# Kernel optimization log

Measured on AMD Instinct MI355X. Metric: run time of the kernel, lower is better.

## Reference

```python
import jax, jax.numpy as jnp
import numpy as np

N = 50000       # nodes
E = 500000      # edges
IN = 128        # in_channels
H = 128         # hidden_channels
R = 8           # num_relations


def setup_inputs() -> dict:
    key = jax.random.key(0)
    ks = jax.random.split(key, 12)
    s_in = 1.0 / np.sqrt(IN)
    s_h = 1.0 / np.sqrt(H)
    return {
        "x": jax.random.normal(ks[0], (N, IN), dtype=jnp.float32),
        "edge_index": jax.random.randint(ks[1], (2, E), 0, N),
        "edge_type": jax.random.randint(ks[2], (E,), 0, R),
        "W1": jax.random.normal(ks[3], (R, IN, H), dtype=jnp.float32) * s_in,
        "root1": jax.random.normal(ks[4], (IN, H), dtype=jnp.float32) * s_in,
        "b1": jnp.zeros((H,), dtype=jnp.float32),
        "W2": jax.random.normal(ks[5], (R, H, H), dtype=jnp.float32) * s_h,
        "root2": jax.random.normal(ks[6], (H, H), dtype=jnp.float32) * s_h,
        "b2": jnp.zeros((H,), dtype=jnp.float32),
        "Wc": jax.random.normal(ks[7], (H, 1), dtype=jnp.float32) * s_h,
        "bc": jnp.zeros((1,), dtype=jnp.float32),
    }


def rgcn_layer(x, W, root, bias, src, dst, etype, num_nodes):
    """PyG RGCNConv (no basis decomposition, aggr='mean', root weight + bias):
    out[i] = x[i] @ root + bias + sum_r mean_{(j->i) in rel r} x[j] @ W[r]
    """
    out = x @ root + bias
    for r in range(W.shape[0]):  # small fixed relation count
        mask = (etype == r).astype(x.dtype)          # [E]
        xr = x @ W[r]                                 # [N, out]
        msg = xr[src] * mask[:, None]                 # gather + mask, [E, out]
        s = jax.ops.segment_sum(msg, dst, num_segments=num_nodes)   # [N, out]
        cnt = jax.ops.segment_sum(mask, dst, num_segments=num_nodes)  # [N]
        out = out + s / jnp.maximum(cnt, 1.0)[:, None]
    return out


def reference(x, edge_index, edge_type, W1, root1, b1, W2, root2, b2, Wc, bc):
    src, dst = edge_index[0], edge_index[1]
    h = jax.nn.relu(rgcn_layer(x, W1, root1, b1, src, dst, edge_type, x.shape[0]))
    # dropout p=0.2 is identity in eval mode
    h = jax.nn.relu(rgcn_layer(h, W2, root2, b2, src, dst, edge_type, x.shape[0]))
    return (h @ Wc + bc)[:, 0]  # squeeze(-1) -> [N]
```

## Files before the change

### kernel.cpp

```cpp
#include <hip/hip_runtime.h>

#define Hd 128
#define LDA 136
#define ZW 1152
#define ZW2 576
#define MAXDEG 64

typedef __attribute__((ext_vector_type(8))) short short8;
typedef __attribute__((ext_vector_type(4))) float f32x4;
typedef __attribute__((ext_vector_type(4))) unsigned int u32x4;

__device__ __forceinline__ unsigned short f2bf(float f) {
    union { float f; unsigned u; } v; v.f = f;
    unsigned r = v.u + 0x7FFFu + ((v.u >> 16) & 1u);
    return (unsigned short)(r >> 16);
}

__global__ __launch_bounds__(256) void prep_kernel(const float* __restrict__ x,
                                                   unsigned short* __restrict__ xbf, int n4,
                                                   const float* __restrict__ root1,
                                                   const float* __restrict__ W1,
                                                   const float* __restrict__ root2,
                                                   const float* __restrict__ W2,
                                                   unsigned short* __restrict__ Bt,
                                                   const int* __restrict__ src,
                                                   const int* __restrict__ dstp,
                                                   const int* __restrict__ et, int E,
                                                   int* __restrict__ deg,
                                                   unsigned int* __restrict__ epk,
                                                   unsigned long long* __restrict__ ovf,
                                                   int* __restrict__ ovfc) {
    const int tid = threadIdx.x;
    if (blockIdx.x < 18) {
        __shared__ float S[32 * 129];
        const int b = blockIdx.x;
        const float* Ws;
        if (b == 0)       Ws = root1;
        else if (b < 9)   Ws = W1 + (size_t)(b - 1) * 16384;
        else if (b == 9)  Ws = root2;
        else              Ws = W2 + (size_t)(b - 10) * 16384;
        unsigned short* Bd = Bt + (size_t)b * 16384;
        for (int s = 0; s < 4; ++s) {
            __syncthreads();
#pragma unroll
            for (int i = 0; i < 16; ++i) {
                int idx = i * 256 + tid;
                int k = idx >> 7, n = idx & 127;
                S[k * 129 + n] = Ws[(size_t)(32 * s + k) * 128 + n];
            }
            __syncthreads();
#pragma unroll
            for (int i = 0; i < 16; ++i) {
                int idx = i * 256 + tid;
                int n = idx >> 5, kk = idx & 31;
                int k = 32 * s + kk;
                int kp = (b >= 9) ? (((k & 15) << 3) | (k >> 4)) : k;
                Bd[n * 128 + kp] = f2bf(S[kk * 129 + n]);
            }
        }
    } else if (blockIdx.x < 18 + 512) {
        const int stride = 512 * 256;
        for (int i = (blockIdx.x - 18) * 256 + tid; i < n4; i += stride) {
            float4 v = ((const float4*)x)[i];
            ushort4 o;
            o.x = f2bf(v.x); o.y = f2bf(v.y); o.z = f2bf(v.z); o.w = f2bf(v.w);
            ((ushort4*)xbf)[i] = o;
        }
    } else {
        int e = (blockIdx.x - 530) * 256 + tid;
        if (e < E) {
            int r = et[e];
            int d = dstp[e];
            int idx = atomicAdd(&deg[d], 1);
            unsigned pay = ((unsigned)src[e] << 3) | (unsigned)r;
            if (idx < MAXDEG) epk[(size_t)d * MAXDEG + idx] = pay;
            else {
                int o = atomicAdd(ovfc, 1);
                ovf[o] = ((unsigned long long)(unsigned)d << 32) | pay;
            }
        }
    }
}

__global__ __launch_bounds__(256, 3) void gemm_z(const unsigned short* __restrict__ A,
                                                 const unsigned short* __restrict__ Bt9,
                                                 unsigned short* __restrict__ z, int M) {
    __shared__ __align__(16) unsigned short As[128 * LDA];
    __shared__ __align__(16) unsigned short Bs[64 * LDA];
    const int tid = threadIdx.x;

    const int nwg = gridDim.x;
    const int nq = nwg >> 3, rr = nwg & 7;
    const int xcd = blockIdx.x & 7, bix = blockIdx.x >> 3;
    const int swz = (xcd < rr ? xcd * (nq + 1) : rr * (nq + 1) + (xcd - rr) * nq) + bix;
    const int mtile = swz / 9, ctile = swz % 9;

    const int rowBase = mtile * 128;
    const int wave = tid >> 6, lane = tid & 63;
    const int lm = lane & 15, lk = (lane >> 4) * 8;
    const unsigned short* Btt = Bt9 + (size_t)ctile * 16384;

#pragma unroll
    for (int i = 0; i < 8; ++i) {
        int idx = i * 256 + tid;
        int r = idx >> 4, c16 = idx & 15;
        int grow = rowBase + r; if (grow >= M) grow = M - 1;
        *(float4*)&As[r * LDA + c16 * 8] = *(const float4*)&A[(size_t)grow * Hd + c16 * 8];
    }
#pragma unroll
    for (int i = 0; i < 4; ++i) {
        int idx = i * 256 + tid;
        *(float4*)&Bs[(idx >> 4) * LDA + (idx & 15) * 8] = *(const float4*)&Btt[idx * 8];
    }

    f32x4 acc[2][8];
#pragma unroll
    for (int mt = 0; mt < 2; ++mt)
#pragma unroll
        for (int nt = 0; nt < 8; ++nt) acc[mt][nt] = (f32x4){0.f, 0.f, 0.f, 0.f};

    __syncthreads();
#pragma unroll
    for (int ks = 0; ks < 4; ++ks) {
        const int k0 = ks * 32 + lk;
        short8 af0 = *(const short8*)&As[(wave * 32 + lm) * LDA + k0];
        short8 af1 = *(const short8*)&As[(wave * 32 + 16 + lm) * LDA + k0];
#pragma unroll
        for (int nt = 0; nt < 4; ++nt) {
            short8 bf = *(const short8*)&Bs[(nt * 16 + lm) * LDA + k0];
            acc[0][nt] = __builtin_amdgcn_mfma_f32_16x16x32_bf16(af0, bf, acc[0][nt], 0, 0, 0);
            acc[1][nt] = __builtin_amdgcn_mfma_f32_16x16x32_bf16(af1, bf, acc[1][nt], 0, 0, 0);
        }
    }
    __syncthreads();
#pragma unroll
    for (int i = 0; i < 4; ++i) {
        int idx = i * 256 + tid;
        *(float4*)&Bs[(idx >> 4) * LDA + (idx & 15) * 8] = *(const float4*)&Btt[(1024 + idx) * 8];
    }
    __syncthreads();
#pragma unroll
    for (int ks = 0; ks < 4; ++ks) {
        const int k0 = ks * 32 + lk;
        short8 af0 = *(const short8*)&As[(wave * 32 + lm) * LDA + k0];
        short8 af1 = *(const short8*)&As[(wave * 32 + 16 + lm) * LDA + k0];
#pragma unroll
        for (int nt = 4; nt < 8; ++nt) {
            short8 bf = *(const short8*)&Bs[((nt - 4) * 16 + lm) * LDA + k0];
            acc[0][nt] = __builtin_amdgcn_mfma_f32_16x16x32_bf16(af0, bf, acc[0][nt], 0, 0, 0);
            acc[1][nt] = __builtin_amdgcn_mfma_f32_16x16x32_bf16(af1, bf, acc[1][nt], 0, 0, 0);
        }
    }

    const int rquad = (lane >> 4) * 4;
#pragma unroll
    for (int mt = 0; mt < 2; ++mt)
#pragma unroll
        for (int reg = 0; reg < 4; ++reg) {
            int row = rowBase + wave * 32 + mt * 16 + rquad + reg;
            if (row >= M) continue;
            u32x4 qv;
#pragma unroll
            for (int j = 0; j < 4; ++j) {
                unsigned lo = f2bf(acc[mt][2 * j][reg]);
                unsigned hi = f2bf(acc[mt][2 * j + 1][reg]);
                qv[j] = lo | (hi << 16);
            }
            *(u32x4*)((char*)z + (size_t)row * (ZW * 2) + ctile * 256 + lm * 16) = qv;
        }
}

__global__ __launch_bounds__(256) void gather_out(const unsigned short* __restrict__ z,
                                                  const int* __restrict__ deg,
                                                  const unsigned int* __restrict__ epk,
                                                  const unsigned long long* __restrict__ ovf,
                                                  const int* __restrict__ ovfc,
                                                  const float* __restrict__ bias,
                                                  const float* __restrict__ Wc,
                                                  const float* __restrict__ bc,
                                                  unsigned short* __restrict__ outb,
                                                  float* __restrict__ outf,
                                                  int N, int mode) {
    const int lane = threadIdx.x & 63;
    const int node = (int)((blockIdx.x * 256 + threadIdx.x) >> 6);
    if (node >= N) return;
    const unsigned int* z32 = (const unsigned int*)z;
    const int half = lane >> 5;
    const int q = lane & 31;

    uint2 vr = *(const uint2*)(z32 + (size_t)node * ZW2 + 2 * q);
    int dt = __builtin_amdgcn_readfirstlane(deg[node]);
    unsigned int ep_v = epk[(size_t)node * MAXDEG + lane];
    const int degc = (dt < MAXDEG) ? dt : MAXDEG;
    const int rel_l = (int)(ep_v & 7u);
    const bool valid = lane < degc;

    int cnt_l = 0;
#pragma unroll
    for (int r = 0; r < 8; ++r) {
        unsigned long long m = __ballot(valid && (rel_l == r));
        int c = (int)__popcll(m);
        if (lane == r) cnt_l = c;
    }
    if (dt > MAXDEG) {
        int oc = __builtin_amdgcn_readfirstlane(ovfc[0]);
        for (int j = 0; j < oc; ++j) {
            unsigned long long v = ovf[j];
            if ((int)(v >> 32) == node && lane == (int)(v & 7u)) cnt_l++;
        }
    }
    float winv = 1.0f / (float)((cnt_l < 1) ? 1 : cnt_l);

    float t0 = 0.f, t1 = 0.f, t2 = 0.f, t3 = 0.f;
#pragma unroll 1
    for (int g = 0; g < degc; g += 16) {
        uint2 vb[8];
        float wb[8];
#pragma unroll
        for (int k = 0; k < 8; ++k) {
            int i = g + 2 * k + half;
            int ic = (i < degc) ? i : (degc - 1);
            unsigned pk = (unsigned)__shfl((int)ep_v, ic);
            int rel = (int)(pk & 7u);
            unsigned base = (pk >> 3) * ZW2 + (unsigned)(rel + 1) * 64;
            vb[k] = *(const uint2*)(z32 + (size_t)base + 2 * q);
            wb[k] = (i < degc) ? __shfl(winv, rel) : 0.f;
        }
#pragma unroll
        for (int k = 0; k < 8; ++k) {
            t0 += wb[k] * __uint_as_float(vb[k].x << 16);
            t1 += wb[k] * __uint_as_float(vb[k].x & 0xffff0000u);
            t2 += wb[k] * __uint_as_float(vb[k].y << 16);
            t3 += wb[k] * __uint_as_float(vb[k].y & 0xffff0000u);
        }
    }
    if (dt > MAXDEG) {
        int oc = __builtin_amdgcn_readfirstlane(ovfc[0]);
        for (int j = 0; j < oc; ++j) {
            unsigned long long v = ovf[j];
            if ((int)(v >> 32) == node) {
                unsigned pk = (unsigned)(v & 0xffffffffu);
                int rel = (int)(pk & 7u);
                unsigned base = (pk >> 3) * ZW2 + (unsigned)(rel + 1) * 64;
                uint2 u = *(const uint2*)(z32 + (size_t)base + 2 * q);
                float w = __shfl(winv, rel);
                if (half == 0) {
                    t0 += w * __uint_as_float(u.x << 16);
                    t1 += w * __uint_as_float(u.x & 0xffff0000u);
                    t2 += w * __uint_as_float(u.y << 16);
                    t3 += w * __uint_as_float(u.y & 0xffff0000u);
                }
            }
        }
    }

    t0 += __shfl_xor(t0, 32);
    t1 += __shfl_xor(t1, 32);
    t2 += __shfl_xor(t2, 32);
    t3 += __shfl_xor(t3, 32);

    const int p0 = 4 * q;
    const int c0 = ((p0 & 7) << 4) + (p0 >> 3);
    const int c1 = (((p0 + 1) & 7) << 4) + ((p0 + 1) >> 3);
    const int c2 = (((p0 + 2) & 7) << 4) + ((p0 + 2) >> 3);
    const int c3 = (((p0 + 3) & 7) << 4) + ((p0 + 3) >> 3);

    t0 = fmaxf(t0 + __uint_as_float(vr.x << 16)         + bias[c0], 0.f);
    t1 = fmaxf(t1 + __uint_as_float(vr.x & 0xffff0000u) + bias[c1], 0.f);
    t2 = fmaxf(t2 + __uint_as_float(vr.y << 16)         + bias[c2], 0.f);
    t3 = fmaxf(t3 + __uint_as_float(vr.y & 0xffff0000u) + bias[c3], 0.f);

    if (mode == 1) {
        if (half == 0) {
            uint2 o;
            o.x = (unsigned)f2bf(t0) | ((unsigned)f2bf(t1) << 16);
            o.y = (unsigned)f2bf(t2) | ((unsigned)f2bf(t3) << 16);
            *(uint2*)((unsigned int*)outb + (size_t)node * 64 + 2 * q) = o;
        }
    } else {
        float s = t0 * Wc[c0] + t1 * Wc[c1] + t2 * Wc[c2] + t3 * Wc[c3];
        s += __shfl_xor(s, 1);
        s += __shfl_xor(s, 2);
        s += __shfl_xor(s, 4);
        s += __shfl_xor(s, 8);
        s += __shfl_xor(s, 16);
        if (lane == 0) outf[node] = s + bc[0];
    }
}

extern "C" void kernel_launch(void* const* d_in, const int* in_sizes, int n_in,
                              void* d_out, int out_size, void* d_ws, size_t ws_size,
                              hipStream_t stream) {
    const float* x     = (const float*)d_in[0];
    const int*   ei    = (const int*)d_in[1];
    const int*   et    = (const int*)d_in[2];
    const float* W1    = (const float*)d_in[3];
    const float* root1 = (const float*)d_in[4];
    const float* b1    = (const float*)d_in[5];
    const float* W2    = (const float*)d_in[6];
    const float* root2 = (const float*)d_in[7];
    const float* b2    = (const float*)d_in[8];
    const float* Wc    = (const float*)d_in[9];
    const float* bc    = (const float*)d_in[10];
    float* out = (float*)d_out;

    const int N = in_sizes[0] / Hd;
    const int E = in_sizes[2];
    const int* src  = ei;
    const int* dstp = ei + E;

    const size_t NH = (size_t)N * Hd;

    size_t off = 0;
    auto carve = [&](size_t bytes) -> char* {
        char* p = (char*)d_ws + off;
        off += (bytes + 255) & ~(size_t)255;
        return p;
    };
    unsigned short* xbf  = (unsigned short*)carve(NH * 2);
    unsigned short* z    = (unsigned short*)carve((size_t)N * ZW * 2);
    unsigned short* Bt   = (unsigned short*)carve((size_t)2 * 9 * 16384 * 2);
    int*            deg  = (int*)carve((size_t)N * 4);
    int*            ovfc = (int*)carve(4);
    unsigned long long* ovf = (unsigned long long*)carve((size_t)E * 8);
    unsigned int*   epk  = (unsigned int*)carve((size_t)N * MAXDEG * 4);
    if (off > ws_size) return;

    size_t zspan = (size_t)((char*)ovfc - (char*)deg) + 256;
    hipMemsetAsync(deg, 0, zspan, stream);

    const int n4 = (int)(NH / 4);
    const int eBlocks = (E + 255) / 256;
    prep_kernel<<<530 + eBlocks, 256, 0, stream>>>(x, xbf, n4, root1, W1, root2, W2, Bt,
                                                   src, dstp, et, E, deg, epk, ovf, ovfc);

    const int Mtiles = (N + 127) / 128;
    const int nodeBlocks = (N + 3) / 4;

    gemm_z<<<Mtiles * 9, 256, 0, stream>>>(xbf, Bt, z, N);
    gather_out<<<nodeBlocks, 256, 0, stream>>>(z, deg, epk, ovf, ovfc, b1, nullptr, nullptr,
                                               xbf, nullptr, N, 1);
    gemm_z<<<Mtiles * 9, 256, 0, stream>>>(xbf, Bt + (size_t)9 * 16384, z, N);
    gather_out<<<nodeBlocks, 256, 0, stream>>>(z, deg, epk, ovf, ovfc, b2, Wc, bc,
                                               nullptr, out, N, 2);
}
```

Measured before the change: 226.3 us.

## Fuse fp32-to-bf16 input conversion into GEMM and skip unused relation stores

After: 264.4 us. +16.8%, slower.

```diff
diff --git a/kernel.cpp b/kernel.cpp
--- a/kernel.cpp
+++ b/kernel.cpp
@@ -16,9 +16,7 @@
     return (unsigned short)(r >> 16);
 }
 
-__global__ __launch_bounds__(256) void prep_kernel(const float* __restrict__ x,
-                                                   unsigned short* __restrict__ xbf, int n4,
-                                                   const float* __restrict__ root1,
+__global__ __launch_bounds__(256) void prep_kernel(const float* __restrict__ root1,
                                                    const float* __restrict__ W1,
                                                    const float* __restrict__ root2,
                                                    const float* __restrict__ W2,
@@ -27,6 +25,7 @@
                                                    const int* __restrict__ dstp,
                                                    const int* __restrict__ et, int E,
                                                    int* __restrict__ deg,
+                                                   int* __restrict__ outmask,
                                                    unsigned int* __restrict__ epk,
                                                    unsigned long long* __restrict__ ovf,
                                                    int* __restrict__ ovfc) {
@@ -58,21 +57,15 @@
                 Bd[n * 128 + kp] = f2bf(S[kk * 129 + n]);
             }
         }
-    } else if (blockIdx.x < 18 + 512) {
-        const int stride = 512 * 256;
-        for (int i = (blockIdx.x - 18) * 256 + tid; i < n4; i += stride) {
-            float4 v = ((const float4*)x)[i];
-            ushort4 o;
-            o.x = f2bf(v.x); o.y = f2bf(v.y); o.z = f2bf(v.z); o.w = f2bf(v.w);
-            ((ushort4*)xbf)[i] = o;
-        }
     } else {
-        int e = (blockIdx.x - 530) * 256 + tid;
+        int e = (blockIdx.x - 18) * 256 + tid;
         if (e < E) {
             int r = et[e];
             int d = dstp[e];
+            int s = src[e];
             int idx = atomicAdd(&deg[d], 1);
-            unsigned pay = ((unsigned)src[e] << 3) | (unsigned)r;
+            atomicOr(&outmask[s], 1 << r);
+            unsigned pay = ((unsigned)s << 3) | (unsigned)r;
             if (idx < MAXDEG) epk[(size_t)d * MAXDEG + idx] = pay;
             else {
                 int o = atomicAdd(ovfc, 1);
@@ -82,8 +75,10 @@
     }
 }
 
-__global__ __launch_bounds__(256, 3) void gemm_z(const unsigned short* __restrict__ A,
+__global__ __launch_bounds__(256, 3) void gemm_z(const unsigned short* __restrict__ Abf,
+                                                 const float* __restrict__ Af32,
                                                  const unsigned short* __restrict__ Bt9,
+                                                 const int* __restrict__ outmask,
                                                  unsigned short* __restrict__ z, int M) {
     __shared__ __align__(16) unsigned short As[128 * LDA];
     __shared__ __align__(16) unsigned short Bs[64 * LDA];
@@ -100,12 +95,28 @@
     const int lm = lane & 15, lk = (lane >> 4) * 8;
     const unsigned short* Btt = Bt9 + (size_t)ctile * 16384;
 
-#pragma unroll
-    for (int i = 0; i < 8; ++i) {
-        int idx = i * 256 + tid;
-        int r = idx >> 4, c16 = idx & 15;
-        int grow = rowBase + r; if (grow >= M) grow = M - 1;
-        *(float4*)&As[r * LDA + c16 * 8] = *(const float4*)&A[(size_t)grow * Hd + c16 * 8];
+    if (Af32) {
+#pragma unroll
+        for (int i = 0; i < 8; ++i) {
+            int idx = i * 256 + tid;
+            int r = idx >> 4, c16 = idx & 15;
+            int grow = rowBase + r; if (grow >= M) grow = M - 1;
+            const float4* px = (const float4*)&Af32[(size_t)grow * Hd + c16 * 8];
+            float4 v0 = px[0], v1 = px[1];
+            ushort4 o0, o1;
+            o0.x = f2bf(v0.x); o0.y = f2bf(v0.y); o0.z = f2bf(v0.z); o0.w = f2bf(v0.w);
+            o1.x = f2bf(v1.x); o1.y = f2bf(v1.y); o1.z = f2bf(v1.z); o1.w = f2bf(v1.w);
+            *(ushort4*)&As[r * LDA + c16 * 8]     = o0;
+            *(ushort4*)&As[r * LDA + c16 * 8 + 4] = o1;
+        }
+    } else {
+#pragma unroll
+        for (int i = 0; i < 8; ++i) {
+            int idx = i * 256 + tid;
+            int r = idx >> 4, c16 = idx & 15;
+            int grow = rowBase + r; if (grow >= M) grow = M - 1;
+            *(float4*)&As[r * LDA + c16 * 8] = *(const float4*)&Abf[(size_t)grow * Hd + c16 * 8];
+        }
     }
 #pragma unroll
     for (int i = 0; i < 4; ++i) {
@@ -159,6 +170,7 @@
         for (int reg = 0; reg < 4; ++reg) {
             int row = rowBase + wave * 32 + mt * 16 + rquad + reg;
             if (row >= M) continue;
+            if (ctile > 0 && !((outmask[row] >> (ctile - 1)) & 1)) continue;
             u32x4 qv;
 #pragma unroll
             for (int j = 0; j < 4; ++j) {
@@ -317,30 +329,30 @@
         off += (bytes + 255) & ~(size_t)255;
         return p;
     };
-    unsigned short* xbf  = (unsigned short*)carve(NH * 2);
-    unsigned short* z    = (unsigned short*)carve((size_t)N * ZW * 2);
-    unsigned short* Bt   = (unsigned short*)carve((size_t)2 * 9 * 16384 * 2);
-    int*            deg  = (int*)carve((size_t)N * 4);
-    int*            ovfc = (int*)carve(4);
+    unsigned short* hbf   = (unsigned short*)carve(NH * 2);
+    unsigned short* z     = (unsigned short*)carve((size_t)N * ZW * 2);
+    unsigned short* Bt    = (unsigned short*)carve((size_t)2 * 9 * 16384 * 2);
+    int*            deg   = (int*)carve((size_t)N * 4);
+    int*            ovfc  = (int*)carve(4);
+    int*            outm  = (int*)carve((size_t)N * 4);
     unsigned long long* ovf = (unsigned long long*)carve((size_t)E * 8);
-    unsigned int*   epk  = (unsigned int*)carve((size_t)N * MAXDEG * 4);
+    unsigned int*   epk   = (unsigned int*)carve((size_t)N * MAXDEG * 4);
     if (off > ws_size) return;
 
-    size_t zspan = (size_t)((char*)ovfc - (char*)deg) + 256;
+    size_t zspan = (size_t)((char*)ovf - (char*)deg);
     hipMemsetAsync(deg, 0, zspan, stream);
 
-    const int n4 = (int)(NH / 4);
     const int eBlocks = (E + 255) / 256;
-    prep_kernel<<<530 + eBlocks, 256, 0, stream>>>(x, xbf, n4, root1, W1, root2, W2, Bt,
-                                                   src, dstp, et, E, deg, epk, ovf, ovfc);
+    prep_kernel<<<18 + eBlocks, 256, 0, stream>>>(root1, W1, root2, W2, Bt,
+                                                  src, dstp, et, E, deg, outm, epk, ovf, ovfc);
 
     const int Mtiles = (N + 127) / 128;
     const int nodeBlocks = (N + 3) / 4;
 
-    gemm_z<<<Mtiles * 9, 256, 0, stream>>>(xbf, Bt, z, N);
+    gemm_z<<<Mtiles * 9, 256, 0, stream>>>(nullptr, x, Bt, outm, z, N);
     gather_out<<<nodeBlocks, 256, 0, stream>>>(z, deg, epk, ovf, ovfc, b1, nullptr, nullptr,
-                                               xbf, nullptr, N, 1);
-    gemm_z<<<Mtiles * 9, 256, 0, stream>>>(xbf, Bt + (size_t)9 * 16384, z, N);
+                                               hbf, nullptr, N, 1);
+    gemm_z<<<Mtiles * 9, 256, 0, stream>>>(hbf, nullptr, Bt + (size_t)9 * 16384, outm, z, N);
     gather_out<<<nodeBlocks, 256, 0, stream>>>(z, deg, epk, ovf, ovfc, b2, Wc, bc,
                                                nullptr, out, N, 2);
 }
```
